# Performance work log

Measured on AMD Instinct MI355X. Metric: run time of the kernel, lower is better.

The kernel has to match this reference:

```python
import jax, jax.numpy as jnp
import numpy as np
import math


def setup_inputs() -> dict:
    key = jax.random.key(0)
    k1, k2, k3 = jax.random.split(key, 3)
    img = jax.random.normal(k1, (32, 3, 512, 512), dtype=jnp.float32)
    c_u = jax.random.normal(k2, (100, 100), dtype=jnp.float32)  # scalar-field mode coeffs for dx
    c_v = jax.random.normal(k3, (100, 100), dtype=jnp.float32)  # scalar-field mode coeffs for dy
    return {"img": img, "c_u": c_u, "c_v": c_v}


def _scalar_field(c, n):
    # random scalar field of size n x n from the first m modes (m = c.shape[0])
    m = c.shape[0]
    x = jnp.linspace(0.0, 1.0, n, dtype=c.dtype)            # [n]
    k = jnp.arange(1, m + 1, dtype=c.dtype)                 # [m]
    i, j = jnp.meshgrid(k, k, indexing='ij')                # [m, m]
    r = jnp.sqrt(i ** 2 + j ** 2)
    e = (r < m + 0.5).astype(c.dtype) / r                   # sqrt(1/energy) per mode
    s = jnp.sin(jnp.pi * x[:, None] * k[None, :])           # [n, m]
    return jnp.einsum('ij,xi,yj->yx', c * e, s, s)          # [n, n]


def reference(img, c_u, c_v):
    n = img.shape[-1]  # square image assumed (n x n)
    m = c_u.shape[0]   # frequency cutoff `cut`

    # temperature_range(n, cut), deterministic T = midpoint of allowed range (alpha=1)
    log_cut = math.log(m + 1e-06)
    T1 = 1.0 / (math.pi * n ** 2 * log_cut)
    T2 = 4.0 / (math.pi ** 3 * m ** 2 * log_cut)
    T2 = max(T1, T2)
    T = 0.5 * (T1 + T2)

    # displacement fields [n, n]
    dx = (T ** 0.5) * _scalar_field(c_u, n) * n
    dy = (T ** 0.5) * _scalar_field(c_v, n) * n

    # remap with bilinear ('linear') interpolation
    dtype = dx.dtype
    y, x = jnp.meshgrid(jnp.arange(n, dtype=dtype), jnp.arange(n, dtype=dtype), indexing='ij')
    xn = jnp.clip(x - dx, 0.0, n - 1)
    yn = jnp.clip(y - dy, 0.0, n - 1)

    xf = jnp.floor(xn).astype(jnp.int32)
    yf = jnp.floor(yn).astype(jnp.int32)
    xc = jnp.ceil(xn).astype(jnp.int32)
    yc = jnp.ceil(yn).astype(jnp.int32)
    xv = xn - xf.astype(dtype)
    yv = yn - yf.astype(dtype)

    out = ((1 - yv) * (1 - xv) * img[..., yf, xf]
           + (1 - yv) * xv * img[..., yf, xc]
           + yv * (1 - xv) * img[..., yc, xf]
           + yv * xv * img[..., yc, xc])
    return out
```

## Files before the change

kernel.cpp:

```cpp
#include <hip/hip_runtime.h>
#include <math.h>

#define NN 512
#define MM 100
#define TPB 256
#define ROWS_OUT 4
#define ROWS_LDS 13
#define PXPT 8

typedef float f32x4 __attribute__((ext_vector_type(4)));


__global__ void sin_table_kernel(float* __restrict__ St) {
    int tid = blockIdx.x * blockDim.x + threadIdx.x;
    if (tid >= NN * MM) return;
    int x = tid / MM, j = tid % MM;
    double arg = M_PI * ((double)x / (double)(NN - 1)) * (double)(j + 1);
    St[tid] = (float)sin(arg);
}

__global__ void bcoef_kernel(const float* __restrict__ St,
                             const float* __restrict__ c_u,
                             const float* __restrict__ c_v,
                             float* __restrict__ B_u,
                             float* __restrict__ B_v) {
    int x = blockIdx.x;
    int j = threadIdx.x;
    if (j >= MM) return;
    float au = 0.f, av = 0.f;
    for (int i = 0; i < MM; ++i) {
        int i1 = i + 1, j1 = j + 1;
        int r2i = i1 * i1 + j1 * j1;
        float w = (r2i <= 10100) ? (1.0f / sqrtf((float)r2i)) : 0.0f;
        float sw = St[x * MM + i] * w;
        au += sw * c_u[i * MM + j];
        av += sw * c_v[i * MM + j];
    }
    B_u[j * NN + x] = au;
    B_v[j * NN + x] = av;
}

#define ROWS_F 4
__global__ __launch_bounds__(256)
void field_kernel(const float* __restrict__ St,
                  const float* __restrict__ B_u,
                  const float* __restrict__ B_v,
                  float scale,
                  float* __restrict__ dx,
                  float* __restrict__ dy) {
    __shared__ float sS[ROWS_F * MM];
    int t = threadIdx.x;
    int y0 = blockIdx.x * ROWS_F;

    for (int i = t; i < ROWS_F * MM; i += 256) {
        int r = i / MM, j = i % MM;
        sS[i] = St[(y0 + r) * MM + j];
    }
    __syncthreads();

    float au[ROWS_F][2] = {}, av[ROWS_F][2] = {};
    for (int j = 0; j < MM; ++j) {
        float bu0 = B_u[j * NN + t], bu1 = B_u[j * NN + t + 256];
        float bv0 = B_v[j * NN + t], bv1 = B_v[j * NN + t + 256];
        #pragma unroll
        for (int r = 0; r < ROWS_F; ++r) {
            float s = sS[r * MM + j];
            au[r][0] += bu0 * s; au[r][1] += bu1 * s;
            av[r][0] += bv0 * s; av[r][1] += bv1 * s;
        }
    }
    #pragma unroll
    for (int r = 0; r < ROWS_F; ++r) {
        int row = (y0 + r) * NN;
        dx[row + t]       = scale * au[r][0];
        dx[row + t + 256] = scale * au[r][1];
        dy[row + t]       = scale * av[r][0];
        dy[row + t + 256] = scale * av[r][1];
    }
}

__global__ __launch_bounds__(TPB, 6)
void remap_kernel(const float* __restrict__ img,
                  const float* __restrict__ dx,
                  const float* __restrict__ dy,
                  float* __restrict__ out,
                  int planes) {
    __shared__ __align__(16) float rows[ROWS_LDS * NN + 1];
    __shared__ int s_mn[4], s_mx[4];

    int nb = gridDim.x;
    int bid = blockIdx.x;
    int sid = (bid & 7) * (nb >> 3) + (bid >> 3);
    int plane = sid >> 7;
    int strip = sid & 127;

    int t = threadIdx.x;
    int Y = strip * ROWS_OUT;

    float w00[PXPT], w01[PXPT], w10[PXPT], w11[PXPT];
    int offA[PXPT], offB[PXPT];
    int myf = NN, Myc = -1;
    #pragma unroll
    for (int i = 0; i < PXPT; ++i) {
        int xi = ((i & 1) << 8) + t;
        int yi = Y + (i >> 1);
        int pix = (yi << 9) + xi;
        float xn = fminf(fmaxf((float)xi - dx[pix], 0.0f), (float)(NN - 1));
        float yn = fminf(fmaxf((float)yi - dy[pix], 0.0f), (float)(NN - 1));
        int xf = (int)floorf(xn), yf = (int)floorf(yn);
        int yc = (int)ceilf(yn);
        float xv = xn - (float)xf, yv = yn - (float)yf;
        w00[i] = (1.f - yv) * (1.f - xv);
        w01[i] = (1.f - yv) * xv;
        w10[i] = yv * (1.f - xv);
        w11[i] = yv * xv;
        offA[i] = (yf << 9) + xf;
        offB[i] = (yc << 9) + xf;
        myf = min(myf, yf);
        Myc = max(Myc, yc);
    }

    for (int d = 32; d; d >>= 1) {
        myf = min(myf, __shfl_xor(myf, d));
        Myc = max(Myc, __shfl_xor(Myc, d));
    }
    int wid = t >> 6;
    if ((t & 63) == 0) { s_mn[wid] = myf; s_mx[wid] = Myc; }
    __syncthreads();
    int r0 = min(min(s_mn[0], s_mn[1]), min(s_mn[2], s_mn[3]));
    int nr = max(max(s_mx[0], s_mx[1]), max(s_mx[2], s_mx[3])) - r0 + 1;

    const float* __restrict__ ip = img + (size_t)plane * (NN * NN);
    float* __restrict__ op = out + (size_t)plane * (NN * NN);

    if (nr <= ROWS_LDS) {
        int rb = r0 << 9;
        #pragma unroll
        for (int i = 0; i < PXPT; ++i) { offA[i] -= rb; offB[i] -= rb; }

        if (t == 0) rows[nr * NN] = 0.f;

        int nbytes = nr << 11;
        int wave = t >> 6;
        int lane_goff = t * 16;
        const char* ipc = (const char*)ip + (rb << 2);
        for (int ob = 0; ob < nbytes; ob += TPB * 16) {
            if (ob + wave * 1024 < nbytes) {
                __builtin_amdgcn_global_load_lds(
                    (const __attribute__((address_space(1))) void*)(ipc + ob + lane_goff),
                    (__attribute__((address_space(3))) void*)((char*)rows + ob + wave * 1024),
                    16, 0, 0);
            }
        }
        __syncthreads();

        #pragma unroll
        for (int i = 0; i < PXPT; ++i) {
            float a0 = rows[offA[i]];
            float a1 = rows[offA[i] + 1];
            float b0 = rows[offB[i]];
            float b1 = rows[offB[i] + 1];
            float o = w00[i] * a0 + w01[i] * a1 + w10[i] * b0 + w11[i] * b1;
            int xi = ((i & 1) << 8) + t;
            int yi = Y + (i >> 1);
            __builtin_nontemporal_store(o, op + (yi << 9) + xi);
        }
    } else {
        #pragma unroll
        for (int i = 0; i < PXPT; ++i) {
            int e1 = ((offA[i] & 511) == 511) ? 0 : 1;
            float a0 = ip[offA[i]], a1 = ip[offA[i] + e1];
            float b0 = ip[offB[i]], b1 = ip[offB[i] + e1];
            float o = w00[i] * a0 + w01[i] * a1 + w10[i] * b0 + w11[i] * b1;
            int xi = ((i & 1) << 8) + t;
            int yi = Y + (i >> 1);
            __builtin_nontemporal_store(o, op + (yi << 9) + xi);
        }
    }
}

extern "C" void kernel_launch(void* const* d_in, const int* in_sizes, int n_in,
                              void* d_out, int out_size, void* d_ws, size_t ws_size,
                              hipStream_t stream) {
    const float* img = (const float*)d_in[0];
    const float* c_u = (const float*)d_in[1];
    const float* c_v = (const float*)d_in[2];
    float* out = (float*)d_out;

    int planes = in_sizes[0] / (NN * NN);

    float* ws  = (float*)d_ws;
    float* St  = ws;
    float* B_u = St  + NN * MM;
    float* B_v = B_u + MM * NN;
    float* dx  = B_v + MM * NN;
    float* dy  = dx  + NN * NN;

    double log_cut = log((double)MM + 1e-6);
    double T1 = 1.0 / (M_PI * (double)NN * (double)NN * log_cut);
    double T2 = 4.0 / (M_PI * M_PI * M_PI * (double)MM * (double)MM * log_cut);
    if (T2 < T1) T2 = T1;
    double T = 0.5 * (T1 + T2);
    float scale = (float)(sqrt(T) * (double)NN);

    sin_table_kernel<<<(NN * MM + 255) / 256, 256, 0, stream>>>(St);
    bcoef_kernel<<<NN, 128, 0, stream>>>(St, c_u, c_v, B_u, B_v);
    field_kernel<<<NN / ROWS_F, 256, 0, stream>>>(St, B_u, B_v, scale, dx, dy);

    int strips = NN / ROWS_OUT;
    remap_kernel<<<strips * planes, TPB, 0, stream>>>(img, dx, dy, out, planes);
}
```

Baseline: 80.10 us.

## Precompute bilinear weights, offsets and strip row ranges once per field, not per plane

The field kernel now computes the per-pixel bilinear weights, relative row offsets and per-strip row range once, and writes them to workspace. The remap kernel, run for all 96 planes, reads these precomputed values instead of recomputing them from dx/dy and doing a block reduction with a barrier. This removes redundant per-plane ALU work and a sync. In exchange, each pixel now loads 24 bytes of weights and offsets instead of 8 bytes of dx/dy, which adds L2 traffic.

Result: slower. 166.6 us (+108.1%).

```diff
diff --git a/kernel.cpp b/kernel.cpp
--- a/kernel.cpp
+++ b/kernel.cpp
@@ -9,6 +9,7 @@
 #define PXPT 8
 
 typedef float f32x4 __attribute__((ext_vector_type(4)));
+typedef int   i32x2 __attribute__((ext_vector_type(2)));
 
 
 __global__ void sin_table_kernel(float* __restrict__ St) {
@@ -40,73 +41,48 @@
     B_v[j * NN + x] = av;
 }
 
-#define ROWS_F 4
 __global__ __launch_bounds__(256)
-void field_kernel(const float* __restrict__ St,
-                  const float* __restrict__ B_u,
-                  const float* __restrict__ B_v,
-                  float scale,
-                  float* __restrict__ dx,
-                  float* __restrict__ dy) {
-    __shared__ float sS[ROWS_F * MM];
+void field_weights_kernel(const float* __restrict__ St,
+                          const float* __restrict__ B_u,
+                          const float* __restrict__ B_v,
+                          float scale,
+                          f32x4* __restrict__ w4,
+                          i32x2* __restrict__ off2,
+                          int* __restrict__ strip_tab) {
+    __shared__ float sS[ROWS_OUT * MM];
+    __shared__ int s_mn[4], s_mx[4];
     int t = threadIdx.x;
-    int y0 = blockIdx.x * ROWS_F;
-
-    for (int i = t; i < ROWS_F * MM; i += 256) {
+    int strip = blockIdx.x;
+    int y0 = strip * ROWS_OUT;
+
+    for (int i = t; i < ROWS_OUT * MM; i += 256) {
         int r = i / MM, j = i % MM;
         sS[i] = St[(y0 + r) * MM + j];
     }
     __syncthreads();
 
-    float au[ROWS_F][2] = {}, av[ROWS_F][2] = {};
+    float au[ROWS_OUT][2] = {}, av[ROWS_OUT][2] = {};
     for (int j = 0; j < MM; ++j) {
         float bu0 = B_u[j * NN + t], bu1 = B_u[j * NN + t + 256];
         float bv0 = B_v[j * NN + t], bv1 = B_v[j * NN + t + 256];
         #pragma unroll
-        for (int r = 0; r < ROWS_F; ++r) {
+        for (int r = 0; r < ROWS_OUT; ++r) {
             float s = sS[r * MM + j];
             au[r][0] += bu0 * s; au[r][1] += bu1 * s;
             av[r][0] += bv0 * s; av[r][1] += bv1 * s;
         }
     }
-    #pragma unroll
-    for (int r = 0; r < ROWS_F; ++r) {
-        int row = (y0 + r) * NN;
-        dx[row + t]       = scale * au[r][0];
-        dx[row + t + 256] = scale * au[r][1];
-        dy[row + t]       = scale * av[r][0];
-        dy[row + t + 256] = scale * av[r][1];
-    }
-}
-
-__global__ __launch_bounds__(TPB, 6)
-void remap_kernel(const float* __restrict__ img,
-                  const float* __restrict__ dx,
-                  const float* __restrict__ dy,
-                  float* __restrict__ out,
-                  int planes) {
-    __shared__ __align__(16) float rows[ROWS_LDS * NN + 1];
-    __shared__ int s_mn[4], s_mx[4];
-
-    int nb = gridDim.x;
-    int bid = blockIdx.x;
-    int sid = (bid & 7) * (nb >> 3) + (bid >> 3);
-    int plane = sid >> 7;
-    int strip = sid & 127;
-
-    int t = threadIdx.x;
-    int Y = strip * ROWS_OUT;
 
     float w00[PXPT], w01[PXPT], w10[PXPT], w11[PXPT];
     int offA[PXPT], offB[PXPT];
     int myf = NN, Myc = -1;
     #pragma unroll
     for (int i = 0; i < PXPT; ++i) {
-        int xi = ((i & 1) << 8) + t;
-        int yi = Y + (i >> 1);
-        int pix = (yi << 9) + xi;
-        float xn = fminf(fmaxf((float)xi - dx[pix], 0.0f), (float)(NN - 1));
-        float yn = fminf(fmaxf((float)yi - dy[pix], 0.0f), (float)(NN - 1));
+        int c = i & 1, r = i >> 1;
+        int xi = (c << 8) + t;
+        int yi = y0 + r;
+        float xn = fminf(fmaxf((float)xi - scale * au[r][c], 0.0f), (float)(NN - 1));
+        float yn = fminf(fmaxf((float)yi - scale * av[r][c], 0.0f), (float)(NN - 1));
         int xf = (int)floorf(xn), yf = (int)floorf(yn);
         int yc = (int)ceilf(yn);
         float xv = xn - (float)xf, yv = yn - (float)yf;
@@ -129,21 +105,49 @@
     __syncthreads();
     int r0 = min(min(s_mn[0], s_mn[1]), min(s_mn[2], s_mn[3]));
     int nr = max(max(s_mx[0], s_mx[1]), max(s_mx[2], s_mx[3])) - r0 + 1;
+    if (t == 0) { strip_tab[2 * strip] = r0; strip_tab[2 * strip + 1] = nr; }
+
+    int rb = r0 << 9;
+    #pragma unroll
+    for (int i = 0; i < PXPT; ++i) {
+        int pix = ((y0 + (i >> 1)) << 9) + ((i & 1) << 8) + t;
+        f32x4 w; w[0] = w00[i]; w[1] = w01[i]; w[2] = w10[i]; w[3] = w11[i];
+        i32x2 o; o[0] = offA[i] - rb; o[1] = offB[i] - rb;
+        w4[pix] = w;
+        off2[pix] = o;
+    }
+}
+
+__global__ __launch_bounds__(TPB, 6)
+void remap_kernel(const float* __restrict__ img,
+                  const f32x4* __restrict__ w4,
+                  const i32x2* __restrict__ off2,
+                  const int* __restrict__ strip_tab,
+                  float* __restrict__ out,
+                  int planes) {
+    __shared__ __align__(16) float rows[ROWS_LDS * NN + 1];
+
+    int nb = gridDim.x;
+    int bid = blockIdx.x;
+    int sid = (bid & 7) * (nb >> 3) + (bid >> 3);
+    int plane = sid >> 7;
+    int strip = sid & 127;
+
+    int t = threadIdx.x;
+    int r0 = strip_tab[2 * strip];
+    int nr = strip_tab[2 * strip + 1];
 
     const float* __restrict__ ip = img + (size_t)plane * (NN * NN);
     float* __restrict__ op = out + (size_t)plane * (NN * NN);
+    int base = ((strip * ROWS_OUT) << 9) + t;
 
     if (nr <= ROWS_LDS) {
-        int rb = r0 << 9;
-        #pragma unroll
-        for (int i = 0; i < PXPT; ++i) { offA[i] -= rb; offB[i] -= rb; }
-
         if (t == 0) rows[nr * NN] = 0.f;
 
         int nbytes = nr << 11;
         int wave = t >> 6;
         int lane_goff = t * 16;
-        const char* ipc = (const char*)ip + (rb << 2);
+        const char* ipc = (const char*)(ip + (r0 << 9));
         for (int ob = 0; ob < nbytes; ob += TPB * 16) {
             if (ob + wave * 1024 < nbytes) {
                 __builtin_amdgcn_global_load_lds(
@@ -156,25 +160,25 @@
 
         #pragma unroll
         for (int i = 0; i < PXPT; ++i) {
-            float a0 = rows[offA[i]];
-            float a1 = rows[offA[i] + 1];
-            float b0 = rows[offB[i]];
-            float b1 = rows[offB[i] + 1];
-            float o = w00[i] * a0 + w01[i] * a1 + w10[i] * b0 + w11[i] * b1;
-            int xi = ((i & 1) << 8) + t;
-            int yi = Y + (i >> 1);
-            __builtin_nontemporal_store(o, op + (yi << 9) + xi);
+            int pix = base + ((i >> 1) << 9) + ((i & 1) << 8);
+            f32x4 w = w4[pix];
+            i32x2 o2 = off2[pix];
+            float o = w[0] * rows[o2[0]] + w[1] * rows[o2[0] + 1]
+                    + w[2] * rows[o2[1]] + w[3] * rows[o2[1] + 1];
+            __builtin_nontemporal_store(o, op + pix);
         }
     } else {
+        int rb = r0 << 9;
         #pragma unroll
         for (int i = 0; i < PXPT; ++i) {
-            int e1 = ((offA[i] & 511) == 511) ? 0 : 1;
-            float a0 = ip[offA[i]], a1 = ip[offA[i] + e1];
-            float b0 = ip[offB[i]], b1 = ip[offB[i] + e1];
-            float o = w00[i] * a0 + w01[i] * a1 + w10[i] * b0 + w11[i] * b1;
-            int xi = ((i & 1) << 8) + t;
-            int yi = Y + (i >> 1);
-            __builtin_nontemporal_store(o, op + (yi << 9) + xi);
+            int pix = base + ((i >> 1) << 9) + ((i & 1) << 8);
+            f32x4 w = w4[pix];
+            i32x2 o2 = off2[pix];
+            int a = o2[0] + rb, b = o2[1] + rb;
+            int e1 = ((a & 511) == 511) ? 0 : 1;
+            float o = w[0] * ip[a] + w[1] * ip[a + e1]
+                    + w[2] * ip[b] + w[3] * ip[b + e1];
+            __builtin_nontemporal_store(o, op + pix);
         }
     }
 }
@@ -189,12 +193,13 @@
 
     int planes = in_sizes[0] / (NN * NN);
 
-    float* ws  = (float*)d_ws;
-    float* St  = ws;
-    float* B_u = St  + NN * MM;
-    float* B_v = B_u + MM * NN;
-    float* dx  = B_v + MM * NN;
-    float* dy  = dx  + NN * NN;
+    float* ws   = (float*)d_ws;
+    float* St   = ws;
+    float* B_u  = St + NN * MM;
+    float* B_v  = B_u + MM * NN;
+    f32x4* w4   = (f32x4*)(ws + 153600);
+    i32x2* off2 = (i32x2*)(ws + 153600 + 4 * NN * NN);
+    int* strip_tab = (int*)(ws + 153600 + 6 * NN * NN);
 
     double log_cut = log((double)MM + 1e-6);
     double T1 = 1.0 / (M_PI * (double)NN * (double)NN * log_cut);
@@ -205,8 +210,10 @@
 
     sin_table_kernel<<<(NN * MM + 255) / 256, 256, 0, stream>>>(St);
     bcoef_kernel<<<NN, 128, 0, stream>>>(St, c_u, c_v, B_u, B_v);
-    field_kernel<<<NN / ROWS_F, 256, 0, stream>>>(St, B_u, B_v, scale, dx, dy);
+    field_weights_kernel<<<NN / ROWS_OUT, 256, 0, stream>>>(St, B_u, B_v, scale,
+                                                            w4, off2, strip_tab);
 
     int strips = NN / ROWS_OUT;
-    remap_kernel<<<strips * planes, TPB, 0, stream>>>(img, dx, dy, out, planes);
-}
+    remap_kernel<<<strips * planes, TPB, 0, stream>>>(img, w4, off2, strip_tab,
+                                                      out, planes);
+}
```
